# Performance work log

Measured on AMD Instinct MI355X. Metric: run time of the kernel, lower is better.

Reference implementation:

```python
import jax, jax.numpy as jnp
import numpy as np

B, N, E, D, H = 1, 100000, 3200000, 16, 128
EPS = 1e-5


def _layer_norm(x, g, b):
    m = jnp.mean(x, axis=-1, keepdims=True)
    v = jnp.mean((x - m) ** 2, axis=-1, keepdims=True)
    return (x - m) * jax.lax.rsqrt(v + EPS) * g + b


def setup_inputs() -> dict:
    key = jax.random.key(0)
    ks = jax.random.split(key, 12)
    inp = {
        "nodes": jax.random.normal(ks[0], (B, N, D), dtype=jnp.float32),
        "edges": jax.random.randint(ks[1], (B, E, 2), 0, N, dtype=jnp.int32),
        "edge_weights": jax.random.uniform(ks[2], (B, E), dtype=jnp.float32),
    }
    dims = [(3 * D, H), (H, H), (H, H), (H, D)]
    for i, (din, dout) in enumerate(dims, start=1):
        inp[f"W{i}"] = jax.random.normal(ks[2 + i], (din, dout), dtype=jnp.float32) * (1.0 / np.sqrt(din))
        inp[f"b{i}"] = jnp.zeros((dout,), dtype=jnp.float32)
        inp[f"g{i}"] = jnp.ones((dout,), dtype=jnp.float32)
        inp[f"be{i}"] = jnp.zeros((dout,), dtype=jnp.float32)
    return inp


def reference(nodes, edges, edge_weights,
              W1, b1, g1, be1, W2, b2, g2, be2,
              W3, b3, g3, be3, W4, b4, g4, be4):
    src = edges[..., 0]  # [B,E]
    dst = edges[..., 1]
    w = edge_weights[..., None]  # [B,E,1]
    # edge-weighted endpoint features
    msg_in = jnp.take_along_axis(nodes, src[..., None], axis=1) * w   # [B,E,D]
    msg_out = jnp.take_along_axis(nodes, dst[..., None], axis=1) * w  # [B,E,D]
    # per-node sum aggregation (scatter-add over edge lists)
    b_idx = jnp.arange(B)[:, None]
    agg_in = jnp.zeros_like(nodes).at[b_idx, dst].add(msg_in)   # in-edges of node i
    agg_out = jnp.zeros_like(nodes).at[b_idx, src].add(msg_out)  # out-edges of node i
    x = jnp.concatenate([agg_in, agg_out, nodes], axis=2)  # [B,N,3D]
    x = jnp.tanh(_layer_norm(x @ W1 + b1, g1, be1))
    x = jnp.tanh(_layer_norm(x @ W2 + b2, g2, be2))
    x = jnp.tanh(_layer_norm(x @ W3 + b3, g3, be3))
    x = jnp.tanh(_layer_norm(x @ W4 + b4, g4, be4))
    return x
```

## Files before the change

### kernel.cpp

```cpp
#include <hip/hip_runtime.h>
#include <stdint.h>

#define DIM 16
#define HID 128
#define TN  32
#define ROWF 132
#define EPSF 1e-5f

__device__ __forceinline__ float safe_tanh(float x) {
    float a = fabsf(x);
    float e = __expf(2.0f * a);
    float t = 1.0f - 2.0f / (e + 1.0f);
    return copysignf(t, x);
}

__global__ void __launch_bounds__(256) edge_scatter_kernel(
    const float* __restrict__ nodes, const int* __restrict__ edges,
    const float* __restrict__ ew, float* __restrict__ agg_in,
    float* __restrict__ agg_out, int nEdges)
{
    int gid = blockIdx.x * 256 + threadIdx.x;
    int e = gid >> 4;
    if (e >= nEdges) return;
    int c = gid & 15;
    int src = edges[2 * e];
    int dst = edges[2 * e + 1];
    float w  = ew[e];
    float vs = nodes[src * DIM + c];
    float vd = nodes[dst * DIM + c];
    atomicAdd(&agg_in[dst * DIM + c], vs * w);
    atomicAdd(&agg_out[src * DIM + c], vd * w);
}

template<int K>
__device__ __forceinline__ void dense_ln_tanh(
    const float* __restrict__ W, const float* __restrict__ bias,
    const float* __restrict__ g, const float* __restrict__ be,
    float (&X)[TN][ROWF], float* mean_s, float* rstd_s, int tid)
{
    const int c0 = (tid & 31) * 4;
    const int n0 = (tid >> 5) * 4;
    float acc[4][4];
    {
        float4 bv = *(const float4*)(bias + c0);
        #pragma unroll
        for (int i = 0; i < 4; ++i) {
            acc[i][0] = bv.x; acc[i][1] = bv.y; acc[i][2] = bv.z; acc[i][3] = bv.w;
        }
    }

    #pragma unroll 2
    for (int k = 0; k < K; k += 4) {
        float xr[4][4];
        #pragma unroll
        for (int i = 0; i < 4; ++i) {
            float4 t = *(const float4*)&X[n0 + i][k];
            xr[i][0] = t.x; xr[i][1] = t.y; xr[i][2] = t.z; xr[i][3] = t.w;
        }
        float w[4][4];
        #pragma unroll
        for (int kk = 0; kk < 4; ++kk) {
            float4 t = *(const float4*)(W + (k + kk) * HID + c0);
            w[kk][0] = t.x; w[kk][1] = t.y; w[kk][2] = t.z; w[kk][3] = t.w;
        }
        #pragma unroll
        for (int kk = 0; kk < 4; ++kk)
            #pragma unroll
            for (int i = 0; i < 4; ++i)
                #pragma unroll
                for (int j = 0; j < 4; ++j) acc[i][j] += xr[i][kk] * w[kk][j];
    }
    __syncthreads();
    #pragma unroll
    for (int i = 0; i < 4; ++i)
        *(float4*)&X[n0 + i][c0] = make_float4(acc[i][0], acc[i][1], acc[i][2], acc[i][3]);
    __syncthreads();

    {
        const int n = tid >> 3;
        const int s = tid & 7;
        float sum = 0.f, sq = 0.f;
        #pragma unroll
        for (int i = 0; i < 16; ++i) {
            float v = X[n][s * 16 + i];
            sum += v; sq += v * v;
        }
        #pragma unroll
        for (int m = 1; m <= 4; m <<= 1) {
            sum += __shfl_xor(sum, m);
            sq  += __shfl_xor(sq, m);
        }
        if (s == 0) {
            float mean = sum * (1.0f / HID);
            float var  = sq * (1.0f / HID) - mean * mean;
            mean_s[n] = mean;
            rstd_s[n] = rsqrtf(fmaxf(var, 0.0f) + EPSF);
        }
    }
    __syncthreads();

    {
        float4 gv  = *(const float4*)(g + c0);
        float4 bev = *(const float4*)(be + c0);
        float gr[4]  = {gv.x, gv.y, gv.z, gv.w};
        float ber[4] = {bev.x, bev.y, bev.z, bev.w};
        #pragma unroll
        for (int i = 0; i < 4; ++i) {
            float m = mean_s[n0 + i], r = rstd_s[n0 + i];
            #pragma unroll
            for (int j = 0; j < 4; ++j)
                acc[i][j] = safe_tanh((acc[i][j] - m) * r * gr[j] + ber[j]);
            *(float4*)&X[n0 + i][c0] = make_float4(acc[i][0], acc[i][1], acc[i][2], acc[i][3]);
        }
    }
    __syncthreads();
}

__global__ void __launch_bounds__(256) mlp_kernel(
    const float* __restrict__ agg_in, const float* __restrict__ agg_out,
    const float* __restrict__ nodes,
    const float* __restrict__ W1, const float* __restrict__ b1, const float* __restrict__ g1, const float* __restrict__ be1,
    const float* __restrict__ W2, const float* __restrict__ b2, const float* __restrict__ g2, const float* __restrict__ be2,
    const float* __restrict__ W3, const float* __restrict__ b3, const float* __restrict__ g3, const float* __restrict__ be3,
    const float* __restrict__ W4, const float* __restrict__ b4, const float* __restrict__ g4, const float* __restrict__ be4,
    float* __restrict__ out, int nNodes)
{
    __shared__ float X[TN][ROWF];
    __shared__ float mean_s[TN], rstd_s[TN];

    const int tid = threadIdx.x;
    const int node0 = blockIdx.x * TN;
    if (node0 >= nNodes) return;

    for (int i = tid; i < TN * 48; i += 256) {
        int n = i / 48, c = i - n * 48;
        int gn = node0 + n;
        float v;
        if (c < 16)      v = agg_in[gn * DIM + c];
        else if (c < 32) v = agg_out[gn * DIM + (c - 16)];
        else             v = nodes[gn * DIM + (c - 32)];
        X[n][c] = v;
    }
    __syncthreads();

    dense_ln_tanh<48>(W1, b1, g1, be1, X, mean_s, rstd_s, tid);
    dense_ln_tanh<128>(W2, b2, g2, be2, X, mean_s, rstd_s, tid);
    dense_ln_tanh<128>(W3, b3, g3, be3, X, mean_s, rstd_s, tid);

    {
        const int c2 = tid & 15;
        const int nn = tid >> 4;
        float aA = b4[c2];
        float aB = aA;
        #pragma unroll 4
        for (int k = 0; k < HID; k += 4) {
            float4 xA = *(const float4*)&X[nn][k];
            float4 xB = *(const float4*)&X[nn + 16][k];
            float xa[4] = {xA.x, xA.y, xA.z, xA.w};
            float xb[4] = {xB.x, xB.y, xB.z, xB.w};
            #pragma unroll
            for (int kk = 0; kk < 4; ++kk) {
                float w = W4[(k + kk) * DIM + c2];
                aA += xa[kk] * w;
                aB += xb[kk] * w;
            }
        }
        float sA = aA, qA = aA * aA, sB = aB, qB = aB * aB;
        #pragma unroll
        for (int m = 1; m <= 8; m <<= 1) {
            sA += __shfl_xor(sA, m); qA += __shfl_xor(qA, m);
            sB += __shfl_xor(sB, m); qB += __shfl_xor(qB, m);
        }
        float g4v = g4[c2], be4v = be4[c2];
        float mA = sA * (1.0f / DIM), vA = fmaxf(qA * (1.0f / DIM) - mA * mA, 0.0f);
        float mB = sB * (1.0f / DIM), vB = fmaxf(qB * (1.0f / DIM) - mB * mB, 0.0f);
        float oA = safe_tanh((aA - mA) * rsqrtf(vA + EPSF) * g4v + be4v);
        float oB = safe_tanh((aB - mB) * rsqrtf(vB + EPSF) * g4v + be4v);
        out[(size_t)(node0 + nn) * DIM + c2]      = oA;
        out[(size_t)(node0 + nn + 16) * DIM + c2] = oB;
    }
}

extern "C" void kernel_launch(void* const* d_in, const int* in_sizes, int n_in,
                              void* d_out, int out_size, void* d_ws, size_t ws_size,
                              hipStream_t stream)
{
    const float* nodes = (const float*)d_in[0];
    const int*   edges = (const int*)d_in[1];
    const float* ew    = (const float*)d_in[2];
    const float *W1 = (const float*)d_in[3],  *b1 = (const float*)d_in[4],
                *g1 = (const float*)d_in[5],  *be1 = (const float*)d_in[6];
    const float *W2 = (const float*)d_in[7],  *b2 = (const float*)d_in[8],
                *g2 = (const float*)d_in[9],  *be2 = (const float*)d_in[10];
    const float *W3 = (const float*)d_in[11], *b3 = (const float*)d_in[12],
                *g3 = (const float*)d_in[13], *be3 = (const float*)d_in[14];
    const float *W4 = (const float*)d_in[15], *b4 = (const float*)d_in[16],
                *g4 = (const float*)d_in[17], *be4 = (const float*)d_in[18];

    const int nNodes = in_sizes[0] / DIM;
    const int nEdges = in_sizes[2];

    float* agg_in  = (float*)d_ws;
    float* agg_out = agg_in + (size_t)nNodes * DIM;

    hipMemsetAsync(d_ws, 0, (size_t)2 * nNodes * DIM * sizeof(float), stream);

    long long ethreads = (long long)nEdges * 16;
    int egrid = (int)((ethreads + 255) / 256);
    edge_scatter_kernel<<<egrid, 256, 0, stream>>>(nodes, edges, ew, agg_in, agg_out, nEdges);

    int mgrid = (nNodes + TN - 1) / TN;
    mlp_kernel<<<mgrid, 256, 0, stream>>>(agg_in, agg_out, nodes,
        W1, b1, g1, be1, W2, b2, g2, be2, W3, b3, g3, be3, W4, b4, g4, be4,
        (float*)d_out, nNodes);
}
```

Before: 581.5 us.

## Replace atomic float scatter with CSR build and gather-based aggregation

Builds per-node in-edge and out-edge lists using a count kernel, an exclusive prefix scan and an atomic fill. A gather kernel then sums weighted neighbor features per node without float atomics. This removes 102M float atomics, but adds several kernel launches, 6.4M integer atomics and a 51 MB list write and read. It falls back to the old scatter path when the workspace is too small.

```diff
diff --git a/kernel.cpp b/kernel.cpp
--- a/kernel.cpp
+++ b/kernel.cpp
@@ -12,6 +12,132 @@
     float e = __expf(2.0f * a);
     float t = 1.0f - 2.0f / (e + 1.0f);
     return copysignf(t, x);
+}
+
+
+__global__ void __launch_bounds__(256) count_kernel(
+    const int* __restrict__ edges, int nEdges, int* __restrict__ cnt, int N)
+{
+    int e = blockIdx.x * 256 + threadIdx.x;
+    if (e >= nEdges) return;
+    int2 sd = ((const int2*)edges)[e];
+    atomicAdd(&cnt[sd.y], 1);
+    atomicAdd(&cnt[N + sd.x], 1);
+}
+
+__global__ void __launch_bounds__(256) block_sums_kernel(
+    const int* __restrict__ in, int n, int* __restrict__ bsum)
+{
+    int i = blockIdx.x * 256 + threadIdx.x;
+    int v = (i < n) ? in[i] : 0;
+    #pragma unroll
+    for (int d = 1; d < 64; d <<= 1) v += __shfl_xor(v, d);
+    __shared__ int ws[4];
+    if ((threadIdx.x & 63) == 0) ws[threadIdx.x >> 6] = v;
+    __syncthreads();
+    if (threadIdx.x == 0) bsum[blockIdx.x] = ws[0] + ws[1] + ws[2] + ws[3];
+}
+
+__global__ void scan_bsums_kernel(int* __restrict__ bsum, int nb)
+{
+    __shared__ int s0[1024], s1[1024];
+    int carry = 0;
+    for (int base = 0; base < nb; base += 1024) {
+        int orig[4];
+        #pragma unroll
+        for (int t = 0; t < 4; ++t) {
+            int i = threadIdx.x + 256 * t;
+            int v = (base + i < nb) ? bsum[base + i] : 0;
+            s0[i] = v; orig[t] = v;
+        }
+        __syncthreads();
+        int* src = s0; int* dst = s1;
+        for (int d = 1; d < 1024; d <<= 1) {
+            #pragma unroll
+            for (int t = 0; t < 4; ++t) {
+                int i = threadIdx.x + 256 * t;
+                dst[i] = src[i] + (i >= d ? src[i - d] : 0);
+            }
+            __syncthreads();
+            int* tmp = src; src = dst; dst = tmp;
+        }
+        #pragma unroll
+        for (int t = 0; t < 4; ++t) {
+            int i = threadIdx.x + 256 * t;
+            if (base + i < nb) bsum[base + i] = carry + src[i] - orig[t];
+        }
+        int total = src[1023];
+        __syncthreads();
+        carry += total;
+    }
+}
+
+__global__ void __launch_bounds__(256) scan_write_kernel(
+    const int* __restrict__ in, int n, const int* __restrict__ bsum,
+    int* __restrict__ out)
+{
+    int i = blockIdx.x * 256 + threadIdx.x;
+    int v = (i < n) ? in[i] : 0;
+    int lane = threadIdx.x & 63, wid = threadIdx.x >> 6;
+    int x = v;
+    #pragma unroll
+    for (int d = 1; d < 64; d <<= 1) {
+        int t = __shfl_up(x, d);
+        if (lane >= d) x += t;
+    }
+    __shared__ int wsum[4], woff[4];
+    if (lane == 63) wsum[wid] = x;
+    __syncthreads();
+    if (threadIdx.x == 0) {
+        int r = 0;
+        #pragma unroll
+        for (int w = 0; w < 4; ++w) { woff[w] = r; r += wsum[w]; }
+    }
+    __syncthreads();
+    if (i < n) out[i] = bsum[blockIdx.x] + woff[wid] + x - v;
+}
+
+__global__ void __launch_bounds__(256) fill_kernel(
+    const int* __restrict__ edges, const float* __restrict__ ew, int nEdges,
+    int* __restrict__ cursor, int N, int2* __restrict__ list)
+{
+    int e = blockIdx.x * 256 + threadIdx.x;
+    if (e >= nEdges) return;
+    int2 sd = ((const int2*)edges)[e];
+    int wb = __float_as_int(ew[e]);
+    int p1 = atomicAdd(&cursor[sd.y], 1);
+    list[p1] = make_int2(sd.x, wb);
+    int p2 = atomicAdd(&cursor[N + sd.x], 1);
+    list[p2] = make_int2(sd.y, wb);
+}
+
+__global__ void __launch_bounds__(256) aggregate_kernel(
+    const float* __restrict__ nodes, const int2* __restrict__ list,
+    const int* __restrict__ offs, const int* __restrict__ cursor,
+    float* __restrict__ agg_in, float* __restrict__ agg_out, int N)
+{
+    int n = blockIdx.x * 4 + (threadIdx.x >> 6);
+    if (n >= N) return;
+    int lane = threadIdx.x & 63;
+    int g = lane >> 4, c = lane & 15;
+
+    float a_in = 0.f, a_out = 0.f;
+    int s = offs[n], e2 = cursor[n];
+    for (int j = s + g; j < e2; j += 4) {
+        int2 ent = list[j];
+        a_in += __int_as_float(ent.y) * nodes[ent.x * DIM + c];
+    }
+    s = offs[N + n]; e2 = cursor[N + n];
+    for (int j = s + g; j < e2; j += 4) {
+        int2 ent = list[j];
+        a_out += __int_as_float(ent.y) * nodes[ent.x * DIM + c];
+    }
+    a_in  += __shfl_xor(a_in, 16);  a_in  += __shfl_xor(a_in, 32);
+    a_out += __shfl_xor(a_out, 16); a_out += __shfl_xor(a_out, 32);
+    if (g == 0) {
+        agg_in[n * DIM + c]  = a_in;
+        agg_out[n * DIM + c] = a_out;
+    }
 }
 
 __global__ void __launch_bounds__(256) edge_scatter_kernel(
@@ -26,10 +152,8 @@
     int src = edges[2 * e];
     int dst = edges[2 * e + 1];
     float w  = ew[e];
-    float vs = nodes[src * DIM + c];
-    float vd = nodes[dst * DIM + c];
-    atomicAdd(&agg_in[dst * DIM + c], vs * w);
-    atomicAdd(&agg_out[src * DIM + c], vd * w);
+    atomicAdd(&agg_in[dst * DIM + c], nodes[src * DIM + c] * w);
+    atomicAdd(&agg_out[src * DIM + c], nodes[dst * DIM + c] * w);
 }
 
 template<int K>
@@ -197,20 +321,54 @@
     const float *W4 = (const float*)d_in[15], *b4 = (const float*)d_in[16],
                 *g4 = (const float*)d_in[17], *be4 = (const float*)d_in[18];
 
-    const int nNodes = in_sizes[0] / DIM;
-    const int nEdges = in_sizes[2];
-
-    float* agg_in  = (float*)d_ws;
-    float* agg_out = agg_in + (size_t)nNodes * DIM;
-
-    hipMemsetAsync(d_ws, 0, (size_t)2 * nNodes * DIM * sizeof(float), stream);
-
-    long long ethreads = (long long)nEdges * 16;
-    int egrid = (int)((ethreads + 255) / 256);
-    edge_scatter_kernel<<<egrid, 256, 0, stream>>>(nodes, edges, ew, agg_in, agg_out, nEdges);
-
-    int mgrid = (nNodes + TN - 1) / TN;
+    const int N = in_sizes[0] / DIM;
+    const int E = in_sizes[2];
+    const int nScan = 2 * N;
+    const int nbScan = (nScan + 255) / 256;
+
+    auto align256 = [](size_t x) { return (x + 255) & ~(size_t)255; };
+    size_t o = 0;
+    size_t agg_in_off  = o; o = align256(o + (size_t)N * DIM * 4);
+    size_t agg_out_off = o; o = align256(o + (size_t)N * DIM * 4);
+    size_t cnt_off     = o; o = align256(o + (size_t)nScan * 4);
+    size_t offs_off    = o; o = align256(o + (size_t)nScan * 4);
+    size_t cursor_off  = o; o = align256(o + (size_t)nScan * 4);
+    size_t bsum_off    = o; o = align256(o + (size_t)nbScan * 4);
+    size_t list_off    = o; o = align256(o + (size_t)2 * E * 8);
+    size_t need = o;
+
+    float* agg_in  = (float*)((char*)d_ws + agg_in_off);
+    float* agg_out = (float*)((char*)d_ws + agg_out_off);
+
+    if (ws_size >= need) {
+        int*  cnt    = (int*)((char*)d_ws + cnt_off);
+        int*  offs   = (int*)((char*)d_ws + offs_off);
+        int*  cursor = (int*)((char*)d_ws + cursor_off);
+        int*  bsum   = (int*)((char*)d_ws + bsum_off);
+        int2* list   = (int2*)((char*)d_ws + list_off);
+
+        hipMemsetAsync(cnt, 0, (size_t)nScan * 4, stream);
+
+        int egrid = (E + 255) / 256;
+        count_kernel<<<egrid, 256, 0, stream>>>(edges, E, cnt, N);
+        block_sums_kernel<<<nbScan, 256, 0, stream>>>(cnt, nScan, bsum);
+        scan_bsums_kernel<<<1, 256, 0, stream>>>(bsum, nbScan);
+        scan_write_kernel<<<nbScan, 256, 0, stream>>>(cnt, nScan, bsum, offs);
+        hipMemcpyAsync(cursor, offs, (size_t)nScan * 4, hipMemcpyDeviceToDevice, stream);
+        fill_kernel<<<egrid, 256, 0, stream>>>(edges, ew, E, cursor, N, list);
+        int agrid = (N + 3) / 4;
+        aggregate_kernel<<<agrid, 256, 0, stream>>>(nodes, list, offs, cursor,
+                                                    agg_in, agg_out, N);
+    } else {
+        hipMemsetAsync(d_ws, 0, (size_t)2 * N * DIM * 4, stream);
+        long long ethreads = (long long)E * 16;
+        int egrid2 = (int)((ethreads + 255) / 256);
+        edge_scatter_kernel<<<egrid2, 256, 0, stream>>>(nodes, edges, ew,
+                                                        agg_in, agg_out, E);
+    }
+
+    int mgrid = (N + TN - 1) / TN;
     mlp_kernel<<<mgrid, 256, 0, stream>>>(agg_in, agg_out, nodes,
         W1, b1, g1, be1, W2, b2, g2, be2, W3, b3, g3, be3, W4, b4, g4, be4,
-        (float*)d_out, nNodes);
-}
+        (float*)d_out, N);
+}
```

Result: slower. 1.270 ms (+118.4%).

## Double MLP node tile and compute LayerNorm stats in registers via shuffles

Applied to the files above, without the earlier changes.

The MLP kernel now processes 64 nodes per block, so each thread holds an 8x4 accumulator tile and reuses every weight load across twice as many rows. LayerNorm mean and variance are reduced directly from registers with cross-lane shuffles across 32 lanes, which removes a shared-memory round trip and two barriers per layer. Input loads use float4 with bounds guards, and the launch bounds request 3 blocks per SM. The larger tile raises register pressure and halves the number of blocks, which could reduce occupancy or cause spills.

```diff
diff --git a/kernel.cpp b/kernel.cpp
--- a/kernel.cpp
+++ b/kernel.cpp
@@ -3,7 +3,7 @@
 
 #define DIM 16
 #define HID 128
-#define TN  32
+#define TN  64
 #define ROWF 132
 #define EPSF 1e-5f
 
@@ -36,24 +36,24 @@
 __device__ __forceinline__ void dense_ln_tanh(
     const float* __restrict__ W, const float* __restrict__ bias,
     const float* __restrict__ g, const float* __restrict__ be,
-    float (&X)[TN][ROWF], float* mean_s, float* rstd_s, int tid)
+    float (&X)[TN][ROWF], int tid)
 {
     const int c0 = (tid & 31) * 4;
-    const int n0 = (tid >> 5) * 4;
-    float acc[4][4];
+    const int n0 = (tid >> 5) * 8;
+    float acc[8][4];
     {
         float4 bv = *(const float4*)(bias + c0);
         #pragma unroll
-        for (int i = 0; i < 4; ++i) {
+        for (int i = 0; i < 8; ++i) {
             acc[i][0] = bv.x; acc[i][1] = bv.y; acc[i][2] = bv.z; acc[i][3] = bv.w;
         }
     }
 
     #pragma unroll 2
     for (int k = 0; k < K; k += 4) {
-        float xr[4][4];
-        #pragma unroll
-        for (int i = 0; i < 4; ++i) {
+        float xr[8][4];
+        #pragma unroll
+        for (int i = 0; i < 8; ++i) {
             float4 t = *(const float4*)&X[n0 + i][k];
             xr[i][0] = t.x; xr[i][1] = t.y; xr[i][2] = t.z; xr[i][3] = t.w;
         }
@@ -66,57 +66,48 @@
         #pragma unroll
         for (int kk = 0; kk < 4; ++kk)
             #pragma unroll
-            for (int i = 0; i < 4; ++i)
+            for (int i = 0; i < 8; ++i)
                 #pragma unroll
                 for (int j = 0; j < 4; ++j) acc[i][j] += xr[i][kk] * w[kk][j];
     }
+
+    float s[8], q[8];
+    #pragma unroll
+    for (int i = 0; i < 8; ++i) {
+        s[i] = acc[i][0] + acc[i][1] + acc[i][2] + acc[i][3];
+        q[i] = acc[i][0]*acc[i][0] + acc[i][1]*acc[i][1]
+             + acc[i][2]*acc[i][2] + acc[i][3]*acc[i][3];
+    }
+    #pragma unroll
+    for (int m = 1; m <= 16; m <<= 1) {
+        #pragma unroll
+        for (int i = 0; i < 8; ++i) {
+            s[i] += __shfl_xor(s[i], m);
+            q[i] += __shfl_xor(q[i], m);
+        }
+    }
+
+    float4 gv  = *(const float4*)(g + c0);
+    float4 bev = *(const float4*)(be + c0);
+    float gr[4]  = {gv.x, gv.y, gv.z, gv.w};
+    float ber[4] = {bev.x, bev.y, bev.z, bev.w};
+
     __syncthreads();
     #pragma unroll
-    for (int i = 0; i < 4; ++i)
-        *(float4*)&X[n0 + i][c0] = make_float4(acc[i][0], acc[i][1], acc[i][2], acc[i][3]);
+    for (int i = 0; i < 8; ++i) {
+        float mean = s[i] * (1.0f / HID);
+        float var  = fmaxf(q[i] * (1.0f / HID) - mean * mean, 0.0f);
+        float r = rsqrtf(var + EPSF);
+        float o[4];
+        #pragma unroll
+        for (int j = 0; j < 4; ++j)
+            o[j] = safe_tanh((acc[i][j] - mean) * r * gr[j] + ber[j]);
+        *(float4*)&X[n0 + i][c0] = make_float4(o[0], o[1], o[2], o[3]);
+    }
     __syncthreads();
-
-    {
-        const int n = tid >> 3;
-        const int s = tid & 7;
-        float sum = 0.f, sq = 0.f;
-        #pragma unroll
-        for (int i = 0; i < 16; ++i) {
-            float v = X[n][s * 16 + i];
-            sum += v; sq += v * v;
-        }
-        #pragma unroll
-        for (int m = 1; m <= 4; m <<= 1) {
-            sum += __shfl_xor(sum, m);
-            sq  += __shfl_xor(sq, m);
-        }
-        if (s == 0) {
-            float mean = sum * (1.0f / HID);
-            float var  = sq * (1.0f / HID) - mean * mean;
-            mean_s[n] = mean;
-            rstd_s[n] = rsqrtf(fmaxf(var, 0.0f) + EPSF);
-        }
-    }
-    __syncthreads();
-
-    {
-        float4 gv  = *(const float4*)(g + c0);
-        float4 bev = *(const float4*)(be + c0);
-        float gr[4]  = {gv.x, gv.y, gv.z, gv.w};
-        float ber[4] = {bev.x, bev.y, bev.z, bev.w};
-        #pragma unroll
-        for (int i = 0; i < 4; ++i) {
-            float m = mean_s[n0 + i], r = rstd_s[n0 + i];
-            #pragma unroll
-            for (int j = 0; j < 4; ++j)
-                acc[i][j] = safe_tanh((acc[i][j] - m) * r * gr[j] + ber[j]);
-            *(float4*)&X[n0 + i][c0] = make_float4(acc[i][0], acc[i][1], acc[i][2], acc[i][3]);
-        }
-    }
-    __syncthreads();
-}
-
-__global__ void __launch_bounds__(256) mlp_kernel(
+}
+
+__global__ void __launch_bounds__(256, 3) mlp_kernel(
     const float* __restrict__ agg_in, const float* __restrict__ agg_out,
     const float* __restrict__ nodes,
     const float* __restrict__ W1, const float* __restrict__ b1, const float* __restrict__ g1, const float* __restrict__ be1,
@@ -126,58 +117,69 @@
     float* __restrict__ out, int nNodes)
 {
     __shared__ float X[TN][ROWF];
-    __shared__ float mean_s[TN], rstd_s[TN];
 
     const int tid = threadIdx.x;
     const int node0 = blockIdx.x * TN;
-    if (node0 >= nNodes) return;
-
-    for (int i = tid; i < TN * 48; i += 256) {
-        int n = i / 48, c = i - n * 48;
+
+    for (int i = tid; i < TN * 12; i += 256) {
+        int n = i / 12, c4 = i - n * 12;
         int gn = node0 + n;
-        float v;
-        if (c < 16)      v = agg_in[gn * DIM + c];
-        else if (c < 32) v = agg_out[gn * DIM + (c - 16)];
-        else             v = nodes[gn * DIM + (c - 32)];
-        X[n][c] = v;
+        float4 v = make_float4(0.f, 0.f, 0.f, 0.f);
+        if (gn < nNodes) {
+            if (c4 < 4)      v = *(const float4*)(agg_in  + gn * DIM + c4 * 4);
+            else if (c4 < 8) v = *(const float4*)(agg_out + gn * DIM + (c4 - 4) * 4);
+            else             v = *(const float4*)(nodes   + gn * DIM + (c4 - 8) * 4);
+        }
+        *(float4*)&X[n][c4 * 4] = v;
     }
     __syncthreads();
 
-    dense_ln_tanh<48>(W1, b1, g1, be1, X, mean_s, rstd_s, tid);
-    dense_ln_tanh<128>(W2, b2, g2, be2, X, mean_s, rstd_s, tid);
-    dense_ln_tanh<128>(W3, b3, g3, be3, X, mean_s, rstd_s, tid);
+    dense_ln_tanh<48>(W1, b1, g1, be1, X, tid);
+    dense_ln_tanh<128>(W2, b2, g2, be2, X, tid);
+    dense_ln_tanh<128>(W3, b3, g3, be3, X, tid);
 
     {
         const int c2 = tid & 15;
-        const int nn = tid >> 4;
-        float aA = b4[c2];
-        float aB = aA;
-        #pragma unroll 4
+        const int nb = tid >> 4;
+        float a[4];
+        {
+            float bv = b4[c2];
+            #pragma unroll
+            for (int t = 0; t < 4; ++t) a[t] = bv;
+        }
+        #pragma unroll 2
         for (int k = 0; k < HID; k += 4) {
-            float4 xA = *(const float4*)&X[nn][k];
-            float4 xB = *(const float4*)&X[nn + 16][k];
-            float xa[4] = {xA.x, xA.y, xA.z, xA.w};
-            float xb[4] = {xB.x, xB.y, xB.z, xB.w};
-            #pragma unroll
-            for (int kk = 0; kk < 4; ++kk) {
-                float w = W4[(k + kk) * DIM + c2];
-                aA += xa[kk] * w;
-                aB += xb[kk] * w;
+            float w[4];
+            #pragma unroll
+            for (int kk = 0; kk < 4; ++kk) w[kk] = W4[(k + kk) * DIM + c2];
+            #pragma unroll
+            for (int t = 0; t < 4; ++t) {
+                float4 x = *(const float4*)&X[nb + 16 * t][k];
+                a[t] += x.x * w[0] + x.y * w[1] + x.z * w[2] + x.w * w[3];
             }
         }
-        float sA = aA, qA = aA * aA, sB = aB, qB = aB * aB;
+        float s[4], q[4];
+        #pragma unroll
+        for (int t = 0; t < 4; ++t) { s[t] = a[t]; q[t] = a[t] * a[t]; }
         #pragma unroll
         for (int m = 1; m <= 8; m <<= 1) {
-            sA += __shfl_xor(sA, m); qA += __shfl_xor(qA, m);
-            sB += __shfl_xor(sB, m); qB += __shfl_xor(qB, m);
+            #pragma unroll
+            for (int t = 0; t < 4; ++t) {
+                s[t] += __shfl_xor(s[t], m);
+                q[t] += __shfl_xor(q[t], m);
+            }
         }
         float g4v = g4[c2], be4v = be4[c2];
-        float mA = sA * (1.0f / DIM), vA = fmaxf(qA * (1.0f / DIM) - mA * mA, 0.0f);
-        float mB = sB * (1.0f / DIM), vB = fmaxf(qB * (1.0f / DIM) - mB * mB, 0.0f);
-        float oA = safe_tanh((aA - mA) * rsqrtf(vA + EPSF) * g4v + be4v);
-        float oB = safe_tanh((aB - mB) * rsqrtf(vB + EPSF) * g4v + be4v);
-        out[(size_t)(node0 + nn) * DIM + c2]      = oA;
-        out[(size_t)(node0 + nn + 16) * DIM + c2] = oB;
+        #pragma unroll
+        for (int t = 0; t < 4; ++t) {
+            int node = node0 + nb + 16 * t;
+            if (node < nNodes) {
+                float mean = s[t] * (1.0f / DIM);
+                float var  = fmaxf(q[t] * (1.0f / DIM) - mean * mean, 0.0f);
+                float o = safe_tanh((a[t] - mean) * rsqrtf(var + EPSF) * g4v + be4v);
+                out[(size_t)node * DIM + c2] = o;
+            }
+        }
     }
 }
 
@@ -197,20 +199,21 @@
     const float *W4 = (const float*)d_in[15], *b4 = (const float*)d_in[16],
                 *g4 = (const float*)d_in[17], *be4 = (const float*)d_in[18];
 
-    const int nNodes = in_sizes[0] / DIM;
-    const int nEdges = in_sizes[2];
+    const int N = in_sizes[0] / DIM;
+    const int E = in_sizes[2];
 
     float* agg_in  = (float*)d_ws;
-    float* agg_out = agg_in + (size_t)nNodes * DIM;
-
-    hipMemsetAsync(d_ws, 0, (size_t)2 * nNodes * DIM * sizeof(float), stream);
-
-    long long ethreads = (long long)nEdges * 16;
+    float* agg_out = agg_in + (size_t)N * DIM;
+
+    hipMemsetAsync(d_ws, 0, (size_t)2 * N * DIM * sizeof(float), stream);
+
+    long long ethreads = (long long)E * 16;
     int egrid = (int)((ethreads + 255) / 256);
-    edge_scatter_kernel<<<egrid, 256, 0, stream>>>(nodes, edges, ew, agg_in, agg_out, nEdges);
-
-    int mgrid = (nNodes + TN - 1) / TN;
+    edge_scatter_kernel<<<egrid, 256, 0, stream>>>(nodes, edges, ew,
+                                                   agg_in, agg_out, E);
+
+    int mgrid = (N + TN - 1) / TN;
     mlp_kernel<<<mgrid, 256, 0, stream>>>(agg_in, agg_out, nodes,
         W1, b1, g1, be1, W2, b2, g2, be2, W3, b3, g3, be3, W4, b4, g4, be4,
-        (float*)d_out, nNodes);
-}
+        (float*)d_out, N);
+}
```

Result: no change. 576.2 us (-0.9%).
